# Performance work log

Hardware: AMD Instinct MI355X
Metric: run time of the kernel (lower is better)

The kernel has to match this reference:

```python
import jax, jax.numpy as jnp
import numpy as np

B, D, H, NT, N_INNER = 512, 32, 128, 64, 8
RTOL, ATOL, DT0, SAFETY = 1e-3, 1e-6, 0.05, 0.9

# Tsit5 (Tsitouras 2011) tableau
C2, C3, C4, C5 = 0.161, 0.327, 0.9, 0.9800255409045097
A21 = 0.161
A31, A32 = -0.008480655492356989, 0.335480655492357
A41, A42, A43 = 2.8971530571054935, -6.359448489975075, 4.3622954328695815
A51, A52, A53, A54 = 5.325864828439257, -11.748883564062828, 7.4955393428898365, -0.09249506636175525
A61, A62, A63, A64, A65 = 5.86145544294642, -12.92096931784711, 8.159367898576159, -0.071584973281401, -0.028269050394068383
B1, B2, B3, B4, B5, B6 = 0.09646076681806523, 0.01, 0.4798896504144996, 1.379008574103742, -3.290069515436081, 2.324710524099774
E1, E2, E3, E4, E5, E6, E7 = -0.0017800110522257771, -0.0008164344596567469, 0.007880878010261995, -0.1447110071732629, 0.5823571654525552, -0.45808210592918697, 0.015151515151515152


def setup_inputs() -> dict:
    key = jax.random.key(0)
    k0, k1, k2 = jax.random.split(key, 3)
    y0 = jax.random.normal(k0, (B, D), jnp.float32)
    ts = (jnp.arange(NT) * 0.1).astype(jnp.float32)
    W1 = jax.random.normal(k1, (D, H), jnp.float32) * 0.1
    b1 = jnp.zeros((H,), jnp.float32)
    W2 = jax.random.normal(k2, (H, D), jnp.float32) * 0.1
    b2 = jnp.zeros((D,), jnp.float32)
    return {"y0": y0, "ts": ts, "W1": W1, "b1": b1, "W2": W2, "b2": b2}


def reference(y0, ts, W1, b1, W2, b2):
    def vf(t, y):  # du/dt = known(t,y) + neural(y); known = -0.5*y
        return -0.5 * y + jnp.tanh(y @ W1 + b1) @ W2 + b2

    def rk_step(t, y, dt, k1):  # one Tsit5 stage-stack, batched over B
        d = dt[:, None]
        k2 = vf(t + C2 * dt, y + d * (A21 * k1))
        k3 = vf(t + C3 * dt, y + d * (A31 * k1 + A32 * k2))
        k4 = vf(t + C4 * dt, y + d * (A41 * k1 + A42 * k2 + A43 * k3))
        k5 = vf(t + C5 * dt, y + d * (A51 * k1 + A52 * k2 + A53 * k3 + A54 * k4))
        k6 = vf(t + dt, y + d * (A61 * k1 + A62 * k2 + A63 * k3 + A64 * k4 + A65 * k5))
        y_new = y + d * (B1 * k1 + B2 * k2 + B3 * k3 + B4 * k4 + B5 * k5 + B6 * k6)
        k7 = vf(t + dt, y_new)  # FSAL
        err = d * (E1 * k1 + E2 * k2 + E3 * k3 + E4 * k4 + E5 * k5 + E6 * k6 + E7 * k7)
        return y_new, k7, err

    def outer_body(carry, t_b):  # integrate adaptively up to save time t_b
        def inner(c, _):
            t, y, dt, k1 = c
            done = t >= t_b - 1e-9
            dtc = jnp.maximum(jnp.minimum(dt, t_b - t), 1e-12)
            y_new, k7, err = rk_step(t, y, dtc, k1)
            tol = ATOL + RTOL * jnp.maximum(jnp.abs(y), jnp.abs(y_new))
            en = jnp.sqrt(jnp.mean((err / tol) ** 2, axis=-1))  # (B,)
            accept = (en <= 1.0) & (~done)
            factor = jnp.clip(SAFETY * jnp.maximum(en, 1e-10) ** -0.2, 0.1, 5.0)
            dt = jnp.where(done, dt, dtc * factor)
            t = jnp.where(accept, t + dtc, t)
            y = jnp.where(accept[:, None], y_new, y)
            k1 = jnp.where(accept[:, None], k7, k1)
            return (t, y, dt, k1), None

        carry, _ = jax.lax.scan(inner, carry, None, length=N_INNER)
        return carry, carry[1]  # save y at t_b

    t0 = jnp.full((B,), ts[0], jnp.float32)
    dt0 = jnp.full((B,), DT0, jnp.float32)
    def vf0(t, y):
        return -0.5 * y + jnp.tanh(y @ W1 + b1) @ W2 + b2
    carry = (t0, y0, dt0, vf0(t0, y0))
    _, ys = jax.lax.scan(outer_body, carry, ts[1:])  # (NT-1, B, D)
    ys = jnp.concatenate([y0[None], ys], axis=0)  # (NT, B, D)
    return jnp.transpose(ys, (1, 0, 2))  # (B, NT, D)
```

## Files before the change

kernel.cpp:

```cpp
#include <hip/hip_runtime.h>

typedef float f32x2 __attribute__((ext_vector_type(2)));
typedef float f32x4 __attribute__((ext_vector_type(4)));

#define NB 512
#define DD 32
#define HH 128
#define NTP 64
#define NINNER 8

__device__ __forceinline__ void pk_fma2(f32x2& acc, f32x2 a, f32x2 b) {
    asm("v_pk_fma_f32 %0, %1, %2, %0" : "+v"(acc) : "v"(a), "v"(b));
}
__device__ __forceinline__ float fexp2(float x) { float r; asm("v_exp_f32 %0, %1" : "=v"(r) : "v"(x)); return r; }
__device__ __forceinline__ float flog2(float x) { float r; asm("v_log_f32 %0, %1" : "=v"(r) : "v"(x)); return r; }
__device__ __forceinline__ float frcpa(float x) { float r; asm("v_rcp_f32 %0, %1" : "=v"(r) : "v"(x)); return r; }

__global__ __launch_bounds__(128, 1)
void ude_kernel(const float* __restrict__ gy0, const float* __restrict__ gts,
                const float* __restrict__ gW1, const float* __restrict__ gb1,
                const float* __restrict__ gW2, const float* __restrict__ gb2,
                float* __restrict__ gout)
{
    constexpr float A21 = 0.161f;
    constexpr float A31 = -0.008480655492356989f, A32 = 0.335480655492357f;
    constexpr float A41 = 2.8971530571054935f, A42 = -6.359448489975075f, A43 = 4.3622954328695815f;
    constexpr float A51 = 5.325864828439257f, A52 = -11.748883564062828f, A53 = 7.4955393428898365f, A54 = -0.09249506636175525f;
    constexpr float A61 = 5.86145544294642f, A62 = -12.92096931784711f, A63 = 8.159367898576159f, A64 = -0.071584973281401f, A65 = -0.028269050394068383f;
    constexpr float B1c = 0.09646076681806523f, B2c = 0.01f, B3c = 0.4798896504144996f,
                    B4c = 1.379008574103742f, B5c = -3.290069515436081f, B6c = 2.324710524099774f;
    constexpr float E1 = -0.001780011052225777f, E2 = -0.0008164344596567469f, E3 = 0.007880878010261995f,
                    E4 = -0.1447110071732629f, E5 = 0.5823571654525552f, E6 = -0.45808210592918697f,
                    E7 = 0.015151515151515152f;

    __shared__ alignas(16) float ybuf[2][64];
    __shared__ alignas(16) float thb[2][HH];

    const int tid = threadIdx.x;
    const int wid = tid >> 6;
    const int l   = tid & 63;
    const int d   = l & 31;
    const int hf  = l >> 5;
    const int e   = blockIdx.x * 2 + wid;

    float* yb = ybuf[wid];
    float* th = thb[wid];

    f32x2 w1a2[16], w1b2[16], w2p[32];
#pragma unroll
    for (int i = 0; i < 16; ++i) {
        w1a2[i][0] = gW1[(2 * i) * HH + l];
        w1a2[i][1] = gW1[(2 * i + 1) * HH + l];
        w1b2[i][0] = gW1[(2 * i) * HH + l + 64];
        w1b2[i][1] = gW1[(2 * i + 1) * HH + l + 64];
    }
#pragma unroll
    for (int j = 0; j < 32; ++j) {
        const int h0 = hf * 64 + 2 * j;
        w2p[j][0] = gW2[h0 * DD + d];
        w2p[j][1] = gW2[(h0 + 1) * DD + d];
    }
    const float bh0 = gb1[l], bh1 = gb1[l + 64], b2d = gb2[d];

    auto ftanh = [](float v) -> float {
        float ex = fexp2(v * 2.885390081777927f);
        return 1.0f - frcpa(ex + 1.0f) * 2.0f;
    };

    auto vf = [&](float ys) -> float {
        yb[l] = ys;
        f32x2 ha = {0.f, 0.f}, hb = {0.f, 0.f}, hc = {0.f, 0.f}, hd = {0.f, 0.f};
        const f32x4* y4 = (const f32x4*)yb;
#pragma unroll
        for (int i = 0; i < 8; ++i) {
            f32x4 v = y4[i];
            f32x2 vlo = {v[0], v[1]}, vhi = {v[2], v[3]};
            pk_fma2(ha, vlo, w1a2[2 * i]);
            pk_fma2(hb, vhi, w1a2[2 * i + 1]);
            pk_fma2(hc, vlo, w1b2[2 * i]);
            pk_fma2(hd, vhi, w1b2[2 * i + 1]);
        }
        const float h0 = bh0 + (ha[0] + ha[1]) + (hb[0] + hb[1]);
        const float h1 = bh1 + (hc[0] + hc[1]) + (hd[0] + hd[1]);
        const float t0 = ftanh(h0);
        const float t1 = ftanh(h1);
        th[l] = t0;
        th[l + 64] = t1;

        f32x2 a0 = {0.f, 0.f}, a1 = {0.f, 0.f}, a2 = {0.f, 0.f}, a3 = {0.f, 0.f};
        const f32x4* t4 = (const f32x4*)(th + (hf << 6));
#pragma unroll
        for (int i = 0; i < 4; ++i) {
            f32x4 va = t4[4 * i + 0], vb = t4[4 * i + 1], vc = t4[4 * i + 2], vd = t4[4 * i + 3];
            pk_fma2(a0, f32x2{va[0], va[1]}, w2p[8 * i + 0]);
            pk_fma2(a0, f32x2{va[2], va[3]}, w2p[8 * i + 1]);
            pk_fma2(a1, f32x2{vb[0], vb[1]}, w2p[8 * i + 2]);
            pk_fma2(a1, f32x2{vb[2], vb[3]}, w2p[8 * i + 3]);
            pk_fma2(a2, f32x2{vc[0], vc[1]}, w2p[8 * i + 4]);
            pk_fma2(a2, f32x2{vc[2], vc[3]}, w2p[8 * i + 5]);
            pk_fma2(a3, f32x2{vd[0], vd[1]}, w2p[8 * i + 6]);
            pk_fma2(a3, f32x2{vd[2], vd[3]}, w2p[8 * i + 7]);
        }
        f32x2 asum = (a0 + a1) + (a2 + a3);
        float s = asum[0] + asum[1];
        s += __shfl_xor(s, 32, 64);
        return fmaf(-0.5f, ys, s + b2d);
    };

    float y  = gy0[e * DD + d];
    float t  = gts[0];
    float dt = 0.05f;
    float k1 = vf(y);

    if (l < 32) gout[e * NTP * DD + l] = y;

#pragma unroll 1
    for (int it = 1; it < NTP; ++it) {
        const float tb = gts[it];
#pragma unroll 1
        for (int s = 0; s < NINNER; ++s) {
            if (t >= tb - 1e-9f) break;

            const float dtc = fmaxf(fminf(dt, tb - t), 1e-12f);

            float st, sx;
            st = fmaf(dtc, A21 * k1, y);
            const float k2 = vf(st);
            sx = fmaf(A32, k2, A31 * k1);
            st = fmaf(dtc, sx, y);
            const float k3 = vf(st);
            sx = A41 * k1; sx = fmaf(A42, k2, sx); sx = fmaf(A43, k3, sx);
            st = fmaf(dtc, sx, y);
            const float k4 = vf(st);
            sx = A51 * k1; sx = fmaf(A52, k2, sx); sx = fmaf(A53, k3, sx); sx = fmaf(A54, k4, sx);
            st = fmaf(dtc, sx, y);
            const float k5 = vf(st);
            sx = A61 * k1; sx = fmaf(A62, k2, sx); sx = fmaf(A63, k3, sx); sx = fmaf(A64, k4, sx); sx = fmaf(A65, k5, sx);
            st = fmaf(dtc, sx, y);
            const float k6 = vf(st);
            sx = B1c * k1; sx = fmaf(B2c, k2, sx); sx = fmaf(B3c, k3, sx);
            sx = fmaf(B4c, k4, sx); sx = fmaf(B5c, k5, sx); sx = fmaf(B6c, k6, sx);
            const float ynew = fmaf(dtc, sx, y);
            const float k7 = vf(ynew);
            sx = E1 * k1; sx = fmaf(E2, k2, sx); sx = fmaf(E3, k3, sx); sx = fmaf(E4, k4, sx);
            sx = fmaf(E5, k5, sx); sx = fmaf(E6, k6, sx); sx = fmaf(E7, k7, sx);
            const float err = dtc * sx;

            const float tol = fmaf(0.001f, fmaxf(fabsf(y), fabsf(ynew)), 1e-06f);
            float q = __fdividef(err, tol);
            q *= q;
#pragma unroll
            for (int m = 1; m <= 16; m <<= 1)
                q += __shfl_xor(q, m, 64);
            const float en2 = q * (1.0f / 32.0f);

            const bool acc = (en2 <= 1.0f);
            float fac = 0.9f * fexp2(-0.1f * flog2(fmaxf(en2, 1e-20f)));
            fac = fminf(fmaxf(fac, 0.1f), 5.0f);

            dt = dtc * fac;
            t  = acc ? (t + dtc) : t;
            y  = acc ? ynew : y;
            k1 = acc ? k7 : k1;
        }
        if (l < 32) gout[e * NTP * DD + it * DD + l] = y;
    }
}

extern "C" void kernel_launch(void* const* d_in, const int* in_sizes, int n_in,
                              void* d_out, int out_size, void* d_ws, size_t ws_size,
                              hipStream_t stream) {
    (void)in_sizes; (void)n_in; (void)out_size; (void)d_ws; (void)ws_size;
    const float* y0 = (const float*)d_in[0];
    const float* ts = (const float*)d_in[1];
    const float* W1 = (const float*)d_in[2];
    const float* b1 = (const float*)d_in[3];
    const float* W2 = (const float*)d_in[4];
    const float* b2 = (const float*)d_in[5];
    ude_kernel<<<dim3(NB / 2), dim3(128), 0, stream>>>(y0, ts, W1, b1, W2, b2, (float*)d_out);
}
```

Measured before the change: 247.6 us.

## Interleave two batch elements per wavefront and use DPP/permlane reductions

Each 64-lane wave now integrates two batch elements together instead of one, interleaving their vector-field evaluations so the two independent dependency chains can overlap and hide latency. Blocks shrink to a single wave. Cross-lane reductions switch from shfl_xor to DPP row ops with a readlane and a permlane32 swap, and the division becomes a reciprocal multiply. The cost is that both elements must step in lockstep until both are done, plus higher register pressure from the duplicated accumulators.

```diff
diff --git a/kernel.cpp b/kernel.cpp
--- a/kernel.cpp
+++ b/kernel.cpp
@@ -16,7 +16,35 @@
 __device__ __forceinline__ float flog2(float x) { float r; asm("v_log_f32 %0, %1" : "=v"(r) : "v"(x)); return r; }
 __device__ __forceinline__ float frcpa(float x) { float r; asm("v_rcp_f32 %0, %1" : "=v"(r) : "v"(x)); return r; }
 
-__global__ __launch_bounds__(128, 1)
+__device__ __forceinline__ float xadd32(float x) {
+#if __has_builtin(__builtin_amdgcn_permlane32_swap)
+    auto r = __builtin_amdgcn_permlane32_swap(__float_as_int(x), __float_as_int(x), false, false);
+    return __int_as_float(r[0]) + __int_as_float(r[1]);
+#else
+    return x + __shfl_xor(x, 32, 64);
+#endif
+}
+
+#define DPP_ADD(s, ctrl) \
+    s += __int_as_float(__builtin_amdgcn_update_dpp(0, __float_as_int(s), ctrl, 0xf, 0xf, true))
+
+__device__ __forceinline__ float wave_sum(float s) {
+#if __has_builtin(__builtin_amdgcn_update_dpp) && __has_builtin(__builtin_amdgcn_readlane)
+    DPP_ADD(s, 0x111);
+    DPP_ADD(s, 0x112);
+    DPP_ADD(s, 0x114);
+    DPP_ADD(s, 0x118);
+    DPP_ADD(s, 0x142);
+    DPP_ADD(s, 0x143);
+    return __int_as_float(__builtin_amdgcn_readlane(__float_as_int(s), 63));
+#else
+#pragma unroll
+    for (int m = 1; m <= 32; m <<= 1) s += __shfl_xor(s, m, 64);
+    return s;
+#endif
+}
+
+__global__ __launch_bounds__(64, 1)
 void ude_kernel(const float* __restrict__ gy0, const float* __restrict__ gts,
                 const float* __restrict__ gW1, const float* __restrict__ gb1,
                 const float* __restrict__ gW2, const float* __restrict__ gb2,
@@ -33,18 +61,14 @@
                     E4 = -0.1447110071732629f, E5 = 0.5823571654525552f, E6 = -0.45808210592918697f,
                     E7 = 0.015151515151515152f;
 
-    __shared__ alignas(16) float ybuf[2][64];
-    __shared__ alignas(16) float thb[2][HH];
-
-    const int tid = threadIdx.x;
-    const int wid = tid >> 6;
-    const int l   = tid & 63;
-    const int d   = l & 31;
-    const int hf  = l >> 5;
-    const int e   = blockIdx.x * 2 + wid;
-
-    float* yb = ybuf[wid];
-    float* th = thb[wid];
+    __shared__ alignas(16) float ybA[64], ybB[64];
+    __shared__ alignas(16) float thA[HH], thB[HH];
+
+    const int l  = threadIdx.x;
+    const int d  = l & 31;
+    const int hf = l >> 5;
+    const int eA = blockIdx.x;
+    const int eB = blockIdx.x + 256;
 
     f32x2 w1a2[16], w1b2[16], w2p[32];
 #pragma unroll
@@ -67,103 +91,155 @@
         return 1.0f - frcpa(ex + 1.0f) * 2.0f;
     };
 
-    auto vf = [&](float ys) -> float {
-        yb[l] = ys;
-        f32x2 ha = {0.f, 0.f}, hb = {0.f, 0.f}, hc = {0.f, 0.f}, hd = {0.f, 0.f};
-        const f32x4* y4 = (const f32x4*)yb;
+    auto vfp = [&](float sAin, float sBin, float& oA, float& oB) {
+        ybA[l] = sAin; ybB[l] = sBin;
+        f32x2 hAa = {0,0}, hAb = {0,0}, hAc = {0,0}, hAd = {0,0};
+        f32x2 hBa = {0,0}, hBb = {0,0}, hBc = {0,0}, hBd = {0,0};
+        const f32x4* yA4 = (const f32x4*)ybA;
+        const f32x4* yB4 = (const f32x4*)ybB;
 #pragma unroll
         for (int i = 0; i < 8; ++i) {
-            f32x4 v = y4[i];
-            f32x2 vlo = {v[0], v[1]}, vhi = {v[2], v[3]};
-            pk_fma2(ha, vlo, w1a2[2 * i]);
-            pk_fma2(hb, vhi, w1a2[2 * i + 1]);
-            pk_fma2(hc, vlo, w1b2[2 * i]);
-            pk_fma2(hd, vhi, w1b2[2 * i + 1]);
+            f32x4 vA = yA4[i], vB = yB4[i];
+            f32x2 vAlo = {vA[0], vA[1]}, vAhi = {vA[2], vA[3]};
+            f32x2 vBlo = {vB[0], vB[1]}, vBhi = {vB[2], vB[3]};
+            pk_fma2(hAa, vAlo, w1a2[2 * i]);
+            pk_fma2(hAb, vAhi, w1a2[2 * i + 1]);
+            pk_fma2(hAc, vAlo, w1b2[2 * i]);
+            pk_fma2(hAd, vAhi, w1b2[2 * i + 1]);
+            pk_fma2(hBa, vBlo, w1a2[2 * i]);
+            pk_fma2(hBb, vBhi, w1a2[2 * i + 1]);
+            pk_fma2(hBc, vBlo, w1b2[2 * i]);
+            pk_fma2(hBd, vBhi, w1b2[2 * i + 1]);
         }
-        const float h0 = bh0 + (ha[0] + ha[1]) + (hb[0] + hb[1]);
-        const float h1 = bh1 + (hc[0] + hc[1]) + (hd[0] + hd[1]);
-        const float t0 = ftanh(h0);
-        const float t1 = ftanh(h1);
-        th[l] = t0;
-        th[l + 64] = t1;
-
-        f32x2 a0 = {0.f, 0.f}, a1 = {0.f, 0.f}, a2 = {0.f, 0.f}, a3 = {0.f, 0.f};
-        const f32x4* t4 = (const f32x4*)(th + (hf << 6));
+        const float hA0 = bh0 + (hAa[0] + hAa[1]) + (hAb[0] + hAb[1]);
+        const float hA1 = bh1 + (hAc[0] + hAc[1]) + (hAd[0] + hAd[1]);
+        const float hB0 = bh0 + (hBa[0] + hBa[1]) + (hBb[0] + hBb[1]);
+        const float hB1 = bh1 + (hBc[0] + hBc[1]) + (hBd[0] + hBd[1]);
+        const float tA0 = ftanh(hA0), tA1 = ftanh(hA1);
+        const float tB0 = ftanh(hB0), tB1 = ftanh(hB1);
+        thA[l] = tA0; thA[l + 64] = tA1;
+        thB[l] = tB0; thB[l + 64] = tB1;
+
+        f32x2 aA0 = {0,0}, aA1 = {0,0}, aA2 = {0,0}, aA3 = {0,0};
+        f32x2 aB0 = {0,0}, aB1 = {0,0}, aB2 = {0,0}, aB3 = {0,0};
+        const f32x4* tA4 = (const f32x4*)(thA + (hf << 6));
+        const f32x4* tB4 = (const f32x4*)(thB + (hf << 6));
 #pragma unroll
         for (int i = 0; i < 4; ++i) {
-            f32x4 va = t4[4 * i + 0], vb = t4[4 * i + 1], vc = t4[4 * i + 2], vd = t4[4 * i + 3];
-            pk_fma2(a0, f32x2{va[0], va[1]}, w2p[8 * i + 0]);
-            pk_fma2(a0, f32x2{va[2], va[3]}, w2p[8 * i + 1]);
-            pk_fma2(a1, f32x2{vb[0], vb[1]}, w2p[8 * i + 2]);
-            pk_fma2(a1, f32x2{vb[2], vb[3]}, w2p[8 * i + 3]);
-            pk_fma2(a2, f32x2{vc[0], vc[1]}, w2p[8 * i + 4]);
-            pk_fma2(a2, f32x2{vc[2], vc[3]}, w2p[8 * i + 5]);
-            pk_fma2(a3, f32x2{vd[0], vd[1]}, w2p[8 * i + 6]);
-            pk_fma2(a3, f32x2{vd[2], vd[3]}, w2p[8 * i + 7]);
+            f32x4 vA0 = tA4[4 * i + 0], vA1 = tA4[4 * i + 1], vA2 = tA4[4 * i + 2], vA3 = tA4[4 * i + 3];
+            f32x4 vB0 = tB4[4 * i + 0], vB1 = tB4[4 * i + 1], vB2 = tB4[4 * i + 2], vB3 = tB4[4 * i + 3];
+            pk_fma2(aA0, f32x2{vA0[0], vA0[1]}, w2p[8 * i + 0]);
+            pk_fma2(aA0, f32x2{vA0[2], vA0[3]}, w2p[8 * i + 1]);
+            pk_fma2(aA1, f32x2{vA1[0], vA1[1]}, w2p[8 * i + 2]);
+            pk_fma2(aA1, f32x2{vA1[2], vA1[3]}, w2p[8 * i + 3]);
+            pk_fma2(aA2, f32x2{vA2[0], vA2[1]}, w2p[8 * i + 4]);
+            pk_fma2(aA2, f32x2{vA2[2], vA2[3]}, w2p[8 * i + 5]);
+            pk_fma2(aA3, f32x2{vA3[0], vA3[1]}, w2p[8 * i + 6]);
+            pk_fma2(aA3, f32x2{vA3[2], vA3[3]}, w2p[8 * i + 7]);
+            pk_fma2(aB0, f32x2{vB0[0], vB0[1]}, w2p[8 * i + 0]);
+            pk_fma2(aB0, f32x2{vB0[2], vB0[3]}, w2p[8 * i + 1]);
+            pk_fma2(aB1, f32x2{vB1[0], vB1[1]}, w2p[8 * i + 2]);
+            pk_fma2(aB1, f32x2{vB1[2], vB1[3]}, w2p[8 * i + 3]);
+            pk_fma2(aB2, f32x2{vB2[0], vB2[1]}, w2p[8 * i + 4]);
+            pk_fma2(aB2, f32x2{vB2[2], vB2[3]}, w2p[8 * i + 5]);
+            pk_fma2(aB3, f32x2{vB3[0], vB3[1]}, w2p[8 * i + 6]);
+            pk_fma2(aB3, f32x2{vB3[2], vB3[3]}, w2p[8 * i + 7]);
         }
-        f32x2 asum = (a0 + a1) + (a2 + a3);
-        float s = asum[0] + asum[1];
-        s += __shfl_xor(s, 32, 64);
-        return fmaf(-0.5f, ys, s + b2d);
+        f32x2 sA2 = (aA0 + aA1) + (aA2 + aA3);
+        f32x2 sB2 = (aB0 + aB1) + (aB2 + aB3);
+        const float sA = xadd32(sA2[0] + sA2[1]);
+        const float sB = xadd32(sB2[0] + sB2[1]);
+        oA = fmaf(-0.5f, sAin, sA + b2d);
+        oB = fmaf(-0.5f, sBin, sB + b2d);
     };
 
-    float y  = gy0[e * DD + d];
-    float t  = gts[0];
-    float dt = 0.05f;
-    float k1 = vf(y);
-
-    if (l < 32) gout[e * NTP * DD + l] = y;
+    float yA = gy0[eA * DD + d], yB = gy0[eB * DD + d];
+    float tA = gts[0],          tB = gts[0];
+    float dtA = 0.05f,          dtB = 0.05f;
+    float k1A, k1B;
+    vfp(yA, yB, k1A, k1B);
+
+    gout[(hf ? eB : eA) * NTP * DD + d] = hf ? yB : yA;
 
 #pragma unroll 1
     for (int it = 1; it < NTP; ++it) {
         const float tb = gts[it];
 #pragma unroll 1
         for (int s = 0; s < NINNER; ++s) {
-            if (t >= tb - 1e-9f) break;
-
-            const float dtc = fmaxf(fminf(dt, tb - t), 1e-12f);
-
-            float st, sx;
-            st = fmaf(dtc, A21 * k1, y);
-            const float k2 = vf(st);
-            sx = fmaf(A32, k2, A31 * k1);
-            st = fmaf(dtc, sx, y);
-            const float k3 = vf(st);
-            sx = A41 * k1; sx = fmaf(A42, k2, sx); sx = fmaf(A43, k3, sx);
-            st = fmaf(dtc, sx, y);
-            const float k4 = vf(st);
-            sx = A51 * k1; sx = fmaf(A52, k2, sx); sx = fmaf(A53, k3, sx); sx = fmaf(A54, k4, sx);
-            st = fmaf(dtc, sx, y);
-            const float k5 = vf(st);
-            sx = A61 * k1; sx = fmaf(A62, k2, sx); sx = fmaf(A63, k3, sx); sx = fmaf(A64, k4, sx); sx = fmaf(A65, k5, sx);
-            st = fmaf(dtc, sx, y);
-            const float k6 = vf(st);
-            sx = B1c * k1; sx = fmaf(B2c, k2, sx); sx = fmaf(B3c, k3, sx);
-            sx = fmaf(B4c, k4, sx); sx = fmaf(B5c, k5, sx); sx = fmaf(B6c, k6, sx);
-            const float ynew = fmaf(dtc, sx, y);
-            const float k7 = vf(ynew);
-            sx = E1 * k1; sx = fmaf(E2, k2, sx); sx = fmaf(E3, k3, sx); sx = fmaf(E4, k4, sx);
-            sx = fmaf(E5, k5, sx); sx = fmaf(E6, k6, sx); sx = fmaf(E7, k7, sx);
-            const float err = dtc * sx;
-
-            const float tol = fmaf(0.001f, fmaxf(fabsf(y), fabsf(ynew)), 1e-06f);
-            float q = __fdividef(err, tol);
-            q *= q;
-#pragma unroll
-            for (int m = 1; m <= 16; m <<= 1)
-                q += __shfl_xor(q, m, 64);
-            const float en2 = q * (1.0f / 32.0f);
-
-            const bool acc = (en2 <= 1.0f);
-            float fac = 0.9f * fexp2(-0.1f * flog2(fmaxf(en2, 1e-20f)));
-            fac = fminf(fmaxf(fac, 0.1f), 5.0f);
-
-            dt = dtc * fac;
-            t  = acc ? (t + dtc) : t;
-            y  = acc ? ynew : y;
-            k1 = acc ? k7 : k1;
+            const bool doneA = (tA >= tb - 1e-9f);
+            const bool doneB = (tB >= tb - 1e-9f);
+            if (doneA && doneB) break;
+
+            const float dtcA = fmaxf(fminf(dtA, tb - tA), 1e-12f);
+            const float dtcB = fmaxf(fminf(dtB, tb - tB), 1e-12f);
+
+            float sxA, sxB, stA, stB;
+            float k2A, k2B, k3A, k3B, k4A, k4B, k5A, k5B, k6A, k6B, k7A, k7B;
+
+            stA = fmaf(dtcA, A21 * k1A, yA);
+            stB = fmaf(dtcB, A21 * k1B, yB);
+            vfp(stA, stB, k2A, k2B);
+
+            sxA = fmaf(A32, k2A, A31 * k1A);
+            sxB = fmaf(A32, k2B, A31 * k1B);
+            stA = fmaf(dtcA, sxA, yA); stB = fmaf(dtcB, sxB, yB);
+            vfp(stA, stB, k3A, k3B);
+
+            sxA = A41 * k1A; sxA = fmaf(A42, k2A, sxA); sxA = fmaf(A43, k3A, sxA);
+            sxB = A41 * k1B; sxB = fmaf(A42, k2B, sxB); sxB = fmaf(A43, k3B, sxB);
+            stA = fmaf(dtcA, sxA, yA); stB = fmaf(dtcB, sxB, yB);
+            vfp(stA, stB, k4A, k4B);
+
+            sxA = A51 * k1A; sxA = fmaf(A52, k2A, sxA); sxA = fmaf(A53, k3A, sxA); sxA = fmaf(A54, k4A, sxA);
+            sxB = A51 * k1B; sxB = fmaf(A52, k2B, sxB); sxB = fmaf(A53, k3B, sxB); sxB = fmaf(A54, k4B, sxB);
+            stA = fmaf(dtcA, sxA, yA); stB = fmaf(dtcB, sxB, yB);
+            vfp(stA, stB, k5A, k5B);
+
+            sxA = A61 * k1A; sxA = fmaf(A62, k2A, sxA); sxA = fmaf(A63, k3A, sxA); sxA = fmaf(A64, k4A, sxA); sxA = fmaf(A65, k5A, sxA);
+            sxB = A61 * k1B; sxB = fmaf(A62, k2B, sxB); sxB = fmaf(A63, k3B, sxB); sxB = fmaf(A64, k4B, sxB); sxB = fmaf(A65, k5B, sxB);
+            stA = fmaf(dtcA, sxA, yA); stB = fmaf(dtcB, sxB, yB);
+            vfp(stA, stB, k6A, k6B);
+
+            sxA = B1c * k1A; sxA = fmaf(B2c, k2A, sxA); sxA = fmaf(B3c, k3A, sxA);
+            sxA = fmaf(B4c, k4A, sxA); sxA = fmaf(B5c, k5A, sxA); sxA = fmaf(B6c, k6A, sxA);
+            sxB = B1c * k1B; sxB = fmaf(B2c, k2B, sxB); sxB = fmaf(B3c, k3B, sxB);
+            sxB = fmaf(B4c, k4B, sxB); sxB = fmaf(B5c, k5B, sxB); sxB = fmaf(B6c, k6B, sxB);
+            const float ynA = fmaf(dtcA, sxA, yA);
+            const float ynB = fmaf(dtcB, sxB, yB);
+            vfp(ynA, ynB, k7A, k7B);
+
+            sxA = E1 * k1A; sxA = fmaf(E2, k2A, sxA); sxA = fmaf(E3, k3A, sxA); sxA = fmaf(E4, k4A, sxA);
+            sxA = fmaf(E5, k5A, sxA); sxA = fmaf(E6, k6A, sxA); sxA = fmaf(E7, k7A, sxA);
+            sxB = E1 * k1B; sxB = fmaf(E2, k2B, sxB); sxB = fmaf(E3, k3B, sxB); sxB = fmaf(E4, k4B, sxB);
+            sxB = fmaf(E5, k5B, sxB); sxB = fmaf(E6, k6B, sxB); sxB = fmaf(E7, k7B, sxB);
+            const float errA = dtcA * sxA;
+            const float errB = dtcB * sxB;
+
+            const float tolA = fmaf(0.001f, fmaxf(fabsf(yA), fabsf(ynA)), 1e-06f);
+            const float tolB = fmaf(0.001f, fmaxf(fabsf(yB), fabsf(ynB)), 1e-06f);
+            float qA = errA * frcpa(tolA); qA *= qA;
+            float qB = errB * frcpa(tolB); qB *= qB;
+            const float enA2 = wave_sum(qA) * (1.0f / 64.0f);
+            const float enB2 = wave_sum(qB) * (1.0f / 64.0f);
+
+            const bool accA = (enA2 <= 1.0f) && !doneA;
+            const bool accB = (enB2 <= 1.0f) && !doneB;
+
+            float fA = 0.9f * fexp2(-0.1f * flog2(fmaxf(enA2, 1e-20f)));
+            float fB = 0.9f * fexp2(-0.1f * flog2(fmaxf(enB2, 1e-20f)));
+            fA = fminf(fmaxf(fA, 0.1f), 5.0f);
+            fB = fminf(fmaxf(fB, 0.1f), 5.0f);
+
+            dtA = doneA ? dtA : dtcA * fA;
+            dtB = doneB ? dtB : dtcB * fB;
+            tA  = accA ? (tA + dtcA) : tA;
+            tB  = accB ? (tB + dtcB) : tB;
+            yA  = accA ? ynA : yA;
+            yB  = accB ? ynB : yB;
+            k1A = accA ? k7A : k1A;
+            k1B = accB ? k7B : k1B;
         }
-        if (l < 32) gout[e * NTP * DD + it * DD + l] = y;
+        gout[(hf ? eB : eA) * NTP * DD + it * DD + d] = hf ? yB : yA;
     }
 }
 
@@ -177,5 +253,5 @@
     const float* b1 = (const float*)d_in[3];
     const float* W2 = (const float*)d_in[4];
     const float* b2 = (const float*)d_in[5];
-    ude_kernel<<<dim3(NB / 2), dim3(128), 0, stream>>>(y0, ts, W1, b1, W2, b2, (float*)d_out);
-}
+    ude_kernel<<<dim3(NB / 2), dim3(64), 0, stream>>>(y0, ts, W1, b1, W2, b2, (float*)d_out);
+}
```

Result: slower. 410.1 us (+65.6%).

## Replace LDS and shuffles with readlane broadcasts, DPP reductions and permlane32 swap

Applied to the files above, without the earlier changes.

The state vector is now broadcast through readlane into scalar values instead of being written to and read back from LDS, and W1 is held as plain scalars with scalar FMAs. The cross-lane reductions are reworked: the error norm uses a DPP row-shift reduction over the whole wave followed by readlane, and the half-wave sum uses permlane32_swap when it is available. Division is replaced by a hardware reciprocal. The aim is to cut LDS round-trips and ds_bpermute latency on the serial vf chain, at the cost of 32 readlanes per evaluation and some scalar-to-vector register traffic.

```diff
diff --git a/kernel.cpp b/kernel.cpp
--- a/kernel.cpp
+++ b/kernel.cpp
@@ -15,6 +15,32 @@
 __device__ __forceinline__ float fexp2(float x) { float r; asm("v_exp_f32 %0, %1" : "=v"(r) : "v"(x)); return r; }
 __device__ __forceinline__ float flog2(float x) { float r; asm("v_log_f32 %0, %1" : "=v"(r) : "v"(x)); return r; }
 __device__ __forceinline__ float frcpa(float x) { float r; asm("v_rcp_f32 %0, %1" : "=v"(r) : "v"(x)); return r; }
+
+__device__ __forceinline__ float rdlane(float x, int i) {
+    return __int_as_float(__builtin_amdgcn_readlane(__float_as_int(x), i));
+}
+
+__device__ __forceinline__ float xadd32(float x) {
+#if __has_builtin(__builtin_amdgcn_permlane32_swap)
+    auto r = __builtin_amdgcn_permlane32_swap(__float_as_int(x), __float_as_int(x), false, false);
+    return __int_as_float(r[0]) + __int_as_float(r[1]);
+#else
+    return x + __shfl_xor(x, 32, 64);
+#endif
+}
+
+#define DPP_ADD(s, ctrl) \
+    s += __int_as_float(__builtin_amdgcn_update_dpp(0, __float_as_int(s), ctrl, 0xf, 0xf, true))
+
+__device__ __forceinline__ float wave_sum(float s) {
+    DPP_ADD(s, 0x111);
+    DPP_ADD(s, 0x112);
+    DPP_ADD(s, 0x114);
+    DPP_ADD(s, 0x118);
+    DPP_ADD(s, 0x142);
+    DPP_ADD(s, 0x143);
+    return rdlane(s, 63);
+}
 
 __global__ __launch_bounds__(128, 1)
 void ude_kernel(const float* __restrict__ gy0, const float* __restrict__ gts,
@@ -33,7 +59,6 @@
                     E4 = -0.1447110071732629f, E5 = 0.5823571654525552f, E6 = -0.45808210592918697f,
                     E7 = 0.015151515151515152f;
 
-    __shared__ alignas(16) float ybuf[2][64];
     __shared__ alignas(16) float thb[2][HH];
 
     const int tid = threadIdx.x;
@@ -43,17 +68,15 @@
     const int hf  = l >> 5;
     const int e   = blockIdx.x * 2 + wid;
 
-    float* yb = ybuf[wid];
     float* th = thb[wid];
 
-    f32x2 w1a2[16], w1b2[16], w2p[32];
-#pragma unroll
-    for (int i = 0; i < 16; ++i) {
-        w1a2[i][0] = gW1[(2 * i) * HH + l];
-        w1a2[i][1] = gW1[(2 * i + 1) * HH + l];
-        w1b2[i][0] = gW1[(2 * i) * HH + l + 64];
-        w1b2[i][1] = gW1[(2 * i + 1) * HH + l + 64];
+    float w1a[DD], w1b[DD];
+#pragma unroll
+    for (int i = 0; i < DD; ++i) {
+        w1a[i] = gW1[i * HH + l];
+        w1b[i] = gW1[i * HH + l + 64];
     }
+    f32x2 w2p[32];
 #pragma unroll
     for (int j = 0; j < 32; ++j) {
         const int h0 = hf * 64 + 2 * j;
@@ -67,44 +90,48 @@
         return 1.0f - frcpa(ex + 1.0f) * 2.0f;
     };
 
-    auto vf = [&](float ys) -> float {
-        yb[l] = ys;
-        f32x2 ha = {0.f, 0.f}, hb = {0.f, 0.f}, hc = {0.f, 0.f}, hd = {0.f, 0.f};
-        const f32x4* y4 = (const f32x4*)yb;
+    auto vf = [&](float st) -> float {
+        float s[DD];
+#pragma unroll
+        for (int i = 0; i < DD; ++i) s[i] = rdlane(st, i);
+
+        float a0 = 0.f, a1 = 0.f, a2 = 0.f, a3 = 0.f;
+        float c0 = 0.f, c1 = 0.f, c2 = 0.f, c3 = 0.f;
 #pragma unroll
         for (int i = 0; i < 8; ++i) {
-            f32x4 v = y4[i];
-            f32x2 vlo = {v[0], v[1]}, vhi = {v[2], v[3]};
-            pk_fma2(ha, vlo, w1a2[2 * i]);
-            pk_fma2(hb, vhi, w1a2[2 * i + 1]);
-            pk_fma2(hc, vlo, w1b2[2 * i]);
-            pk_fma2(hd, vhi, w1b2[2 * i + 1]);
+            a0 = fmaf(s[4 * i + 0], w1a[4 * i + 0], a0);
+            a1 = fmaf(s[4 * i + 1], w1a[4 * i + 1], a1);
+            a2 = fmaf(s[4 * i + 2], w1a[4 * i + 2], a2);
+            a3 = fmaf(s[4 * i + 3], w1a[4 * i + 3], a3);
+            c0 = fmaf(s[4 * i + 0], w1b[4 * i + 0], c0);
+            c1 = fmaf(s[4 * i + 1], w1b[4 * i + 1], c1);
+            c2 = fmaf(s[4 * i + 2], w1b[4 * i + 2], c2);
+            c3 = fmaf(s[4 * i + 3], w1b[4 * i + 3], c3);
         }
-        const float h0 = bh0 + (ha[0] + ha[1]) + (hb[0] + hb[1]);
-        const float h1 = bh1 + (hc[0] + hc[1]) + (hd[0] + hd[1]);
+        const float h0 = bh0 + ((a0 + a1) + (a2 + a3));
+        const float h1 = bh1 + ((c0 + c1) + (c2 + c3));
         const float t0 = ftanh(h0);
         const float t1 = ftanh(h1);
         th[l] = t0;
         th[l + 64] = t1;
 
-        f32x2 a0 = {0.f, 0.f}, a1 = {0.f, 0.f}, a2 = {0.f, 0.f}, a3 = {0.f, 0.f};
+        f32x2 p0 = {0.f, 0.f}, p1 = {0.f, 0.f}, p2 = {0.f, 0.f}, p3 = {0.f, 0.f};
         const f32x4* t4 = (const f32x4*)(th + (hf << 6));
 #pragma unroll
         for (int i = 0; i < 4; ++i) {
             f32x4 va = t4[4 * i + 0], vb = t4[4 * i + 1], vc = t4[4 * i + 2], vd = t4[4 * i + 3];
-            pk_fma2(a0, f32x2{va[0], va[1]}, w2p[8 * i + 0]);
-            pk_fma2(a0, f32x2{va[2], va[3]}, w2p[8 * i + 1]);
-            pk_fma2(a1, f32x2{vb[0], vb[1]}, w2p[8 * i + 2]);
-            pk_fma2(a1, f32x2{vb[2], vb[3]}, w2p[8 * i + 3]);
-            pk_fma2(a2, f32x2{vc[0], vc[1]}, w2p[8 * i + 4]);
-            pk_fma2(a2, f32x2{vc[2], vc[3]}, w2p[8 * i + 5]);
-            pk_fma2(a3, f32x2{vd[0], vd[1]}, w2p[8 * i + 6]);
-            pk_fma2(a3, f32x2{vd[2], vd[3]}, w2p[8 * i + 7]);
+            pk_fma2(p0, f32x2{va[0], va[1]}, w2p[8 * i + 0]);
+            pk_fma2(p0, f32x2{va[2], va[3]}, w2p[8 * i + 1]);
+            pk_fma2(p1, f32x2{vb[0], vb[1]}, w2p[8 * i + 2]);
+            pk_fma2(p1, f32x2{vb[2], vb[3]}, w2p[8 * i + 3]);
+            pk_fma2(p2, f32x2{vc[0], vc[1]}, w2p[8 * i + 4]);
+            pk_fma2(p2, f32x2{vc[2], vc[3]}, w2p[8 * i + 5]);
+            pk_fma2(p3, f32x2{vd[0], vd[1]}, w2p[8 * i + 6]);
+            pk_fma2(p3, f32x2{vd[2], vd[3]}, w2p[8 * i + 7]);
         }
-        f32x2 asum = (a0 + a1) + (a2 + a3);
-        float s = asum[0] + asum[1];
-        s += __shfl_xor(s, 32, 64);
-        return fmaf(-0.5f, ys, s + b2d);
+        f32x2 ps = (p0 + p1) + (p2 + p3);
+        const float ssum = xadd32(ps[0] + ps[1]);
+        return fmaf(-0.5f, st, ssum + b2d);
     };
 
     float y  = gy0[e * DD + d];
@@ -126,33 +153,36 @@
             float st, sx;
             st = fmaf(dtc, A21 * k1, y);
             const float k2 = vf(st);
+
             sx = fmaf(A32, k2, A31 * k1);
             st = fmaf(dtc, sx, y);
             const float k3 = vf(st);
+
             sx = A41 * k1; sx = fmaf(A42, k2, sx); sx = fmaf(A43, k3, sx);
             st = fmaf(dtc, sx, y);
             const float k4 = vf(st);
+
             sx = A51 * k1; sx = fmaf(A52, k2, sx); sx = fmaf(A53, k3, sx); sx = fmaf(A54, k4, sx);
             st = fmaf(dtc, sx, y);
             const float k5 = vf(st);
+
             sx = A61 * k1; sx = fmaf(A62, k2, sx); sx = fmaf(A63, k3, sx); sx = fmaf(A64, k4, sx); sx = fmaf(A65, k5, sx);
             st = fmaf(dtc, sx, y);
             const float k6 = vf(st);
+
             sx = B1c * k1; sx = fmaf(B2c, k2, sx); sx = fmaf(B3c, k3, sx);
             sx = fmaf(B4c, k4, sx); sx = fmaf(B5c, k5, sx); sx = fmaf(B6c, k6, sx);
             const float ynew = fmaf(dtc, sx, y);
             const float k7 = vf(ynew);
+
             sx = E1 * k1; sx = fmaf(E2, k2, sx); sx = fmaf(E3, k3, sx); sx = fmaf(E4, k4, sx);
             sx = fmaf(E5, k5, sx); sx = fmaf(E6, k6, sx); sx = fmaf(E7, k7, sx);
             const float err = dtc * sx;
 
             const float tol = fmaf(0.001f, fmaxf(fabsf(y), fabsf(ynew)), 1e-06f);
-            float q = __fdividef(err, tol);
+            float q = err * frcpa(tol);
             q *= q;
-#pragma unroll
-            for (int m = 1; m <= 16; m <<= 1)
-                q += __shfl_xor(q, m, 64);
-            const float en2 = q * (1.0f / 32.0f);
+            const float en2 = wave_sum(q) * (1.0f / 64.0f);
 
             const bool acc = (en2 <= 1.0f);
             float fac = 0.9f * fexp2(-0.1f * flog2(fmaxf(en2, 1e-20f)));
```

New measurement: 223.6 us. 9.7% less time.
